# Optimization experiments

Measured on AMD Instinct MI355X. Metric: run time of the kernel, lower is better.

The kernel has to match this reference:

```python
import jax, jax.numpy as jnp
import numpy as np

EPS = 1e-7
BLOCK_SIZE = 128
LN_EPS = 1e-6

def _project(x):
    norm = jnp.maximum(jnp.linalg.norm(x, axis=-1, keepdims=True), EPS)
    max_norm = 1.0 - EPS
    return jnp.where(norm >= 1.0, x / norm * max_norm, x)

def _mobius_add(x, y, c):
    x2 = jnp.sum(x * x, -1, keepdims=True)
    y2 = jnp.sum(y * y, -1, keepdims=True)
    xy = jnp.sum(x * y, -1, keepdims=True)
    num = (1 + 2 * c * xy + c * y2) * x + (1 - c * x2) * y
    den = 1 + 2 * c * xy + c * c * x2 * y2
    return _project(num / jnp.maximum(den, EPS))

def _logmap0(y, c):
    sqrt_c = jnp.maximum(jnp.sqrt(c), EPS)
    y_norm = jnp.linalg.norm(y, axis=-1, keepdims=True)
    safe = jnp.maximum(y_norm, EPS)
    mag = jnp.arctanh(jnp.minimum(y_norm, 1.0 - EPS)) / sqrt_c
    return jnp.where(y_norm < EPS, jnp.zeros_like(y), mag * (y / safe))

def _expmap0(v, c):
    sqrt_c = jnp.maximum(jnp.sqrt(c), EPS)
    v_norm = jnp.linalg.norm(v, axis=-1, keepdims=True)
    safe = jnp.maximum(v_norm, EPS)
    mag = jnp.tanh(sqrt_c * safe) / sqrt_c
    return _project(jnp.where(v_norm < EPS, jnp.zeros_like(v), mag * (v / safe)))

def _dist(x, y, c):
    sqrt_c = jnp.maximum(jnp.sqrt(c), EPS)
    add_norm = jnp.linalg.norm(_mobius_add(-x, y, c), axis=-1)
    sc = jnp.squeeze(sqrt_c, -1)
    arg = jnp.minimum(sc * add_norm, 1.0 - EPS)
    return 2.0 * jnp.arctanh(arg) / sc

def _layernorm(t, scale, bias):
    mu = jnp.mean(t, -1, keepdims=True)
    var = jnp.mean((t - mu) ** 2, -1, keepdims=True)
    return (t - mu) * jax.lax.rsqrt(var + LN_EPS) * scale + bias

def _rope(x, fc):
    # x: [Be, H, bs, hd]; fc: [bs, hd//2] complex
    x_r, x_i = jnp.split(x, 2, -1)
    xc = jax.lax.complex(x_r, x_i)
    rot = xc * fc.reshape(1, 1, fc.shape[0], fc.shape[1])
    return jnp.concatenate([rot.real, rot.imag], -1)

def setup_inputs() -> dict:
    key = jax.random.key(0)
    ks = jax.random.split(key, 8)
    B, N, D, H = 1, 1024, 1024, 16
    w = lambda k, s: jax.random.normal(k, s, jnp.float32) * 0.02
    x = jax.random.normal(ks[0], (B, N, D), jnp.float32) * 0.02  # points inside the ball
    c_global = jax.random.uniform(ks[1], (B, 1), jnp.float32, minval=0.1, maxval=1.0)
    return dict(
        x=x, c_global=c_global,
        qkv_w=w(ks[2], (D, 3 * D)), qkv_b=jnp.zeros((3 * D,), jnp.float32),
        out_w=w(ks[3], (D, D)), out_b=jnp.zeros((D,), jnp.float32),
        ffn_w1=w(ks[4], (D, 4 * D)), ffn_b1=jnp.zeros((4 * D,), jnp.float32),
        ffn_w2=w(ks[5], (4 * D, D)), ffn_b2=jnp.zeros((D,), jnp.float32),
        ln1_scale=jnp.ones((D,), jnp.float32), ln1_bias=jnp.zeros((D,), jnp.float32),
        ln2_scale=jnp.ones((D,), jnp.float32), ln2_bias=jnp.zeros((D,), jnp.float32),
        c_logits=jnp.zeros((H,), jnp.float32),
        geo_scale=jnp.ones((1, H, 1, 1), jnp.float32),
        start_pos=0,
    )

def reference(x, c_global, qkv_w, qkv_b, out_w, out_b, ffn_w1, ffn_b1, ffn_w2, ffn_b2,
              ln1_scale, ln1_bias, ln2_scale, ln2_bias, c_logits, geo_scale, start_pos):
    B, N, D = x.shape
    H = c_logits.shape[0]
    hd = D // H
    bs = BLOCK_SIZE
    nb = N // bs
    Be = B * nb
    xb = x.reshape(Be, bs, D)
    c_b = jnp.repeat(c_global, nb, axis=0).reshape(Be, 1, 1)
    x_res1 = xb
    # tangent-space norm 1 + attention input
    x_norm = _expmap0(_layernorm(_logmap0(xb, c_b), ln1_scale, ln1_bias), c_b)
    x_tan = _logmap0(x_norm, c_b)
    qkv = (x_tan @ qkv_w + qkv_b).reshape(Be, bs, 3, H, hd).transpose(2, 0, 3, 1, 4)
    q, k, v = qkv[0], qkv[1], qkv[2]  # [Be, H, bs, hd]
    # block-local RoPE (module recomputes freqs_cis for h_dim/block_size internally)
    freqs = 1.0 / (10000.0 ** (jnp.arange(0, hd, 2, dtype=jnp.float32) / hd))
    fc = jnp.exp(1j * jnp.outer(jnp.arange(bs), freqs))
    q = _rope(q, fc)
    k = _rope(k, fc)
    c_head = jax.nn.softplus(c_logits).reshape(1, H, 1, 1)
    q_hyp = _expmap0(q, c_head)
    k_hyp = _expmap0(k, c_head)
    d = _dist(q_hyp[:, :, :, None, :], k_hyp[:, :, None, :, :], c_head[:, :, None, :, :])  # [Be,H,bs,bs]
    attn = jax.nn.softmax(-geo_scale * d, axis=-1)
    ao = jnp.einsum('bhqk,bhkd->bhqd', attn, v).transpose(0, 2, 1, 3).reshape(Be, bs, D)
    ao = ao @ out_w + out_b
    x_att = _mobius_add(x_res1, _expmap0(ao, c_b), c_b)
    # tangent-space norm 2 + hyperbolic FFN
    x_norm2 = _expmap0(_layernorm(_logmap0(x_att, c_b), ln2_scale, ln2_bias), c_b)
    t = _logmap0(x_norm2, c_b)
    t = jax.nn.gelu(t @ ffn_w1 + ffn_b1) @ ffn_w2 + ffn_b2
    x_ffn = _expmap0(t, c_b)
    out = _mobius_add(x_att, x_ffn, c_b)
    return out.reshape(B, N, D)
```

## Files before the change

### kernel.cpp

```cpp
#include <hip/hip_runtime.h>

typedef unsigned int uint;
typedef unsigned short ushort;
typedef __attribute__((ext_vector_type(8))) short bf16x8;
typedef __attribute__((ext_vector_type(4))) float f32x4;

#define EPSF 1e-7f
#define ONE_M_EPS 0.99999988079071044921875f
#define ATANH_1ME 8.4056213f
#define Y2_CLIP 0.99999982f

__device__ __forceinline__ ushort f2bf(float f){
  union{float f;uint u;}x; x.f=f; uint u=x.u;
  return (ushort)((u + 0x7fffu + ((u>>16)&1u)) >> 16);
}
__device__ __forceinline__ float bf2f(ushort u){
  union{uint u;float f;}x; x.u = ((uint)u)<<16; return x.f;
}
__device__ __forceinline__ float atanh_c(float a){
  a = fminf(a, ONE_M_EPS);
  return 0.5f*__logf((1.f+a)/(1.f-a));
}
__device__ __forceinline__ float gelu_t(float v){
  return 0.5f*v*(1.f + tanhf(0.7978845608f*(v + 0.044715f*v*v*v)));
}

__device__ __forceinline__ float expmap_factor(float n2, float sc, float& r2){
  float n = sqrtf(n2);
  if (n < EPSF) { r2 = 0.f; return 0.f; }
  float mag = tanhf(sc*n)/sc;
  float f = mag/n;
  if (mag >= 1.f) { f *= ONE_M_EPS/mag; r2 = Y2_CLIP; }
  else r2 = mag*mag;
  return f;
}
__device__ __forceinline__ float roundtrip_factor(float tn2, float sc){
  float tn = sqrtf(tn2);
  if (tn < EPSF) return 0.f;
  float mag = tanhf(sc*tn)/sc;
  if (mag >= 1.f) {
    return ATANH_1ME / (sc * tn);
  } else {
    if (mag < EPSF) return 0.f;
    return (mag/tn) * (atanh_c(mag) / (sc * mag));
  }
}

__device__ __constant__ float FREQS[32] = {
  1.0f, 0.7498942093324559f, 0.5623413251903491f, 0.4216965034285822f,
  0.31622776601683794f, 0.23713737056616552f, 0.1778279410038923f, 0.13335214321633242f,
  0.1f, 0.07498942093324558f, 0.05623413251903491f, 0.04216965034285822f,
  0.03162277660168379f, 0.023713737056616554f, 0.01778279410038923f, 0.013335214321633242f,
  0.01f, 0.007498942093324559f, 0.005623413251903491f, 0.004216965034285822f,
  0.0031622776601683794f, 0.0023713737056616554f, 0.0017782794100389228f, 0.0013335214321633241f,
  0.001f, 0.0007498942093324558f, 0.0005623413251903491f, 0.0004216965034285822f,
  0.00031622776601683794f, 0.00023713737056616553f, 0.00017782794100389227f, 0.00013335214321633243f
};

__device__ __forceinline__ float blkSum(float v, float* tmp){
  #pragma unroll
  for (int o=32;o>0;o>>=1) v += __shfl_xor(v, o, 64);
  int w = threadIdx.x >> 6;
  if ((threadIdx.x & 63) == 0) tmp[w] = v;
  __syncthreads();
  v = tmp[0]+tmp[1]+tmp[2]+tmp[3];
  __syncthreads();
  return v;
}
__device__ __forceinline__ float2 blkSum2(float a, float b, float* tmp){
  #pragma unroll
  for (int o=32;o>0;o>>=1){ a += __shfl_xor(a, o, 64); b += __shfl_xor(b, o, 64); }
  int w = threadIdx.x >> 6;
  if ((threadIdx.x & 63) == 0){ tmp[w] = a; tmp[4+w] = b; }
  __syncthreads();
  float2 r; r.x = tmp[0]+tmp[1]+tmp[2]+tmp[3]; r.y = tmp[4]+tmp[5]+tmp[6]+tmp[7];
  __syncthreads();
  return r;
}

__global__ __launch_bounds__(256) void k_pre(const float* __restrict__ qkv_w,
    const float* __restrict__ out_w, const float* __restrict__ ffn_w1,
    const float* __restrict__ ffn_w2, const float* __restrict__ x,
    const float* __restrict__ cg, const float* __restrict__ lns, const float* __restrict__ lnb,
    ushort* __restrict__ wq, ushort* __restrict__ wo,
    ushort* __restrict__ w1, ushort* __restrict__ w2, ushort* __restrict__ xtan){
  __shared__ float s[32][33];
  int b = blockIdx.x;
  if (b < 12288){
    const float* W; ushort* WT; int K, N;
    if (b < 3072){ W=qkv_w; WT=wq; K=1024; N=3072; }
    else if (b < 4096){ b-=3072; W=out_w; WT=wo; K=1024; N=1024; }
    else if (b < 8192){ b-=4096; W=ffn_w1; WT=w1; K=1024; N=4096; }
    else { b-=8192; W=ffn_w2; WT=w2; K=4096; N=1024; }
    int nbn = N >> 5;
    int n0 = (b % nbn)*32, k0 = (b / nbn)*32;
    int tx = threadIdx.x & 31, ty = threadIdx.x >> 5;
    #pragma unroll
    for (int i=0;i<4;i++)
      s[ty+8*i][tx] = W[(size_t)(k0+ty+8*i)*N + n0+tx];
    __syncthreads();
    #pragma unroll
    for (int i=0;i<4;i++)
      WT[(size_t)(n0+ty+8*i)*K + k0+tx] = f2bf(s[tx][ty+8*i]);
  } else {
    float* tmp = &s[0][0];
    int r = b - 12288, t = threadIdx.x;
    float c = cg[0];
    float sc = fmaxf(sqrtf(c), EPSF);
    float4 xv = ((const float4*)(x + (size_t)r*1024))[t];
    float n2 = blkSum(xv.x*xv.x + xv.y*xv.y + xv.z*xv.z + xv.w*xv.w, tmp);
    float n = sqrtf(n2);
    float f1 = (n < EPSF) ? 0.f : (atanh_c(n) / sc / n);
    float ux = xv.x*f1, uy = xv.y*f1, uz = xv.z*f1, uw = xv.w*f1;
    float2 s12 = blkSum2(ux+uy+uz+uw, ux*ux+uy*uy+uz*uz+uw*uw, tmp);
    float mu = s12.x*(1.f/1024.f);
    float var = s12.y*(1.f/1024.f) - mu*mu;
    float inv = rsqrtf(var + 1e-6f);
    float4 sv = ((const float4*)lns)[t];
    float4 bv = ((const float4*)lnb)[t];
    float ta = (ux-mu)*inv*sv.x + bv.x;
    float tb = (uy-mu)*inv*sv.y + bv.y;
    float tc = (uz-mu)*inv*sv.z + bv.z;
    float td = (uw-mu)*inv*sv.w + bv.w;
    float tn2 = blkSum(ta*ta+tb*tb+tc*tc+td*td, tmp);
    float f = roundtrip_factor(tn2, sc);
    ushort4 o; o.x=f2bf(ta*f); o.y=f2bf(tb*f); o.z=f2bf(tc*f); o.w=f2bf(td*f);
    ((ushort4*)(xtan + (size_t)r*1024))[t] = o;
  }
}

template<int EPI>
__global__ __launch_bounds__(256) void k_gemm(const ushort* __restrict__ A,
    const ushort* __restrict__ Bt, const float* __restrict__ bias,
    void* __restrict__ C, int M, int N, int Kstride, int Kchunk,
    ushort* __restrict__ qhg, ushort* __restrict__ qlg,
    ushort* __restrict__ khg, ushort* __restrict__ klg,
    ushort* __restrict__ vhg, float* __restrict__ q2g, float* __restrict__ k2g,
    const float* __restrict__ clog){
  constexpr int MF = 2, NF = 4;
  __shared__ ushort As[2][128*64];
  __shared__ ushort Bs[2][64*64];
  const int tid = threadIdx.x;
  const int lane = tid & 63;
  const int wid = tid >> 6;
  const int ro = wid * 32;
  const int l15 = lane & 15, hi = lane >> 4;
  const int nwg = gridDim.x * gridDim.y;
  const int lin = blockIdx.y * gridDim.x + blockIdx.x;
  const int qq = nwg >> 3, rr = nwg & 7;
  const int xcd = lin & 7, ii = lin >> 3;
  const int swz = (xcd < rr) ? (xcd*(qq+1) + ii) : (rr*(qq+1) + (xcd-rr)*qq + ii);
  const int m0 = (swz % gridDim.y) * 128;
  const int n0 = (swz / gridDim.y) * 64;
  const int z = blockIdx.z;
  const int kbase = z * Kchunk;
  const int swr = (l15 & 7) << 3;

  f32x4 acc[MF][NF];
  #pragma unroll
  for (int i=0;i<MF;i++)
    #pragma unroll
    for (int j=0;j<NF;j++) acc[i][j] = (f32x4){0.f,0.f,0.f,0.f};

  auto stage = [&](int buf, int koff){
    #pragma unroll
    for (int r2=0;r2<4;r2++){
      int idx = r2*256 + tid;
      int row = idx >> 3, cc = idx & 7;
      int off = koff + ((cc ^ (row & 7)) << 3);
      const ushort* ga = A + (size_t)(m0+row)*Kstride + off;
      int lo = (r2*256 + (tid & 192)) * 8;
      __builtin_amdgcn_global_load_lds((const __attribute__((address_space(1))) uint*)ga,
          (__attribute__((address_space(3))) uint*)&As[buf][lo], 16, 0, 0);
    }
    #pragma unroll
    for (int r2=0;r2<2;r2++){
      int idx = r2*256 + tid;
      int row = idx >> 3, cc = idx & 7;
      int off = koff + ((cc ^ (row & 7)) << 3);
      const ushort* gb = Bt + (size_t)(n0+row)*Kstride + off;
      int lo = (r2*256 + (tid & 192)) * 8;
      __builtin_amdgcn_global_load_lds((const __attribute__((address_space(1))) uint*)gb,
          (__attribute__((address_space(3))) uint*)&Bs[buf][lo], 16, 0, 0);
    }
  };
  auto compute = [&](int buf){
    #pragma unroll
    for (int ks=0;ks<2;ks++){
      bf16x8 af[MF], bfv[NF];
      int cb = (ks*32 + hi*8) ^ swr;
      #pragma unroll
      for (int m2=0;m2<MF;m2++) af[m2]  = *(const bf16x8*)&As[buf][(ro+m2*16+l15)*64 + cb];
      #pragma unroll
      for (int n2=0;n2<NF;n2++) bfv[n2] = *(const bf16x8*)&Bs[buf][(n2*16+l15)*64 + cb];
      #pragma unroll
      for (int m2=0;m2<MF;m2++)
        #pragma unroll
        for (int n2=0;n2<NF;n2++)
          acc[m2][n2] = __builtin_amdgcn_mfma_f32_16x16x32_bf16(af[m2], bfv[n2], acc[m2][n2], 0, 0, 0);
    }
  };

  const int nt = Kchunk >> 6;
  stage(0, kbase);
  __syncthreads();
  int cur = 0;
  for (int t = 1; t < nt; ++t){
    stage(cur ^ 1, kbase + t*64);
    compute(cur);
    __syncthreads();
    cur ^= 1;
  }
  compute(cur);

  if (EPI == 4){
    float v[MF][NF][4];
    #pragma unroll
    for (int m2=0;m2<MF;m2++)
      #pragma unroll
      for (int n2=0;n2<NF;n2++){
        float bb = bias[n0 + n2*16 + l15];
        #pragma unroll
        for (int i=0;i<4;i++) v[m2][n2][i] = acc[m2][n2][i] + bb;
      }
    const int type = n0 >> 10;
    const int h = (n0 & 1023) >> 6;
    if (type < 2){
      #pragma unroll
      for (int m2=0;m2<MF;m2++)
        #pragma unroll
        for (int i=0;i<4;i++){
          int gr = m0 + ro + m2*16 + hi*4 + i;
          float r = (float)(gr & 127);
          #pragma unroll
          for (int pp=0;pp<2;pp++){
            int d = pp*16 + l15;
            float sn, cn; __sincosf(r * FREQS[d], &sn, &cn);
            float a = v[m2][pp][i], b = v[m2][pp+2][i];
            v[m2][pp][i]   = a*cn - b*sn;
            v[m2][pp+2][i] = a*sn + b*cn;
          }
        }
      const float cl = clog[h];
      const float chh = (cl > 20.f) ? cl : log1pf(__expf(cl));
      const float sch = fmaxf(sqrtf(chh), EPSF);
      ushort* hdst = (type==0) ? qhg : khg;
      ushort* ldst = (type==0) ? qlg : klg;
      float*  sdst = (type==0) ? q2g : k2g;
      #pragma unroll
      for (int m2=0;m2<MF;m2++)
        #pragma unroll
        for (int i=0;i<4;i++){
          float n2s = 0.f;
          #pragma unroll
          for (int n2=0;n2<NF;n2++) n2s += v[m2][n2][i]*v[m2][n2][i];
          #pragma unroll
          for (int o=1;o<16;o<<=1) n2s += __shfl_xor(n2s, o);
          float r2; float f = expmap_factor(n2s, sch, r2);
          int gr = m0 + ro + m2*16 + hi*4 + i;
          int be = gr >> 7, r = gr & 127;
          size_t rowbase = ((size_t)(be*16 + h)*128 + r)*64;
          #pragma unroll
          for (int n2=0;n2<NF;n2++){
            float val = v[m2][n2][i]*f;
            ushort hb = f2bf(val);
            ushort lb = f2bf(val - bf2f(hb));
            hdst[rowbase + n2*16 + l15] = hb;
            ldst[rowbase + n2*16 + l15] = lb;
          }
          if (l15 == 0) sdst[(size_t)(be*16+h)*128 + r] = r2;
        }
    } else {
      #pragma unroll
      for (int m2=0;m2<MF;m2++)
        #pragma unroll
        for (int i=0;i<4;i++){
          int gr = m0 + ro + m2*16 + hi*4 + i;
          int be = gr >> 7, r = gr & 127;
          size_t rowbase = ((size_t)(be*16 + h)*128 + r)*64;
          #pragma unroll
          for (int n2=0;n2<NF;n2++)
            vhg[rowbase + n2*16 + l15] = f2bf(v[m2][n2][i]);
        }
    }
    return;
  }

  #pragma unroll
  for (int m=0;m<MF;m++){
    #pragma unroll
    for (int n=0;n<NF;n++){
      int gc = n0 + n*16 + l15;
      float bb = (EPI == 3) ? (z == 0 ? bias[gc] : 0.f) : bias[gc];
      #pragma unroll
      for (int i=0;i<4;i++){
        int gr = m0 + ro + m*16 + hi*4 + i;
        float v2 = acc[m][n][i] + bb;
        if (EPI == 2) v2 = gelu_t(v2);
        if (EPI == 2) ((ushort*)C)[(size_t)gr*N + gc] = f2bf(v2);
        else ((float*)C)[(size_t)z*M*N + (size_t)gr*N + gc] = v2;
      }
    }
  }
}

__global__ __launch_bounds__(256) void k_attn6(const ushort* __restrict__ qhg,
    const ushort* __restrict__ qlg, const ushort* __restrict__ khg,
    const ushort* __restrict__ klg, const ushort* __restrict__ vhg,
    const float* __restrict__ q2g, const float* __restrict__ k2g,
    const float* __restrict__ c_logits, const float* __restrict__ geo,
    ushort* __restrict__ ao){
  __shared__ ushort Kh[128*64], Kl[128*64];
  __shared__ ushort Vth[64*128];
  __shared__ ushort Qh[64*64], Ql[64*64];
  __shared__ float k2s[128], q2s[64];
  const int h = blockIdx.x, be = blockIdx.y, qs = blockIdx.z;
  const int tid = threadIdx.x;
  const float cl = c_logits[h];
  const float ch = (cl > 20.f) ? cl : log1pf(__expf(cl));
  const float sc = fmaxf(sqrtf(ch), EPSF);
  const float gs = geo[h];
  const size_t tbase = (size_t)(be*16 + h)*8192;

  #pragma unroll
  for (int r2=0;r2<4;r2++){
    int idx = r2*256 + tid;
    int row = idx >> 3, cc = idx & 7;
    int off = row*64 + ((cc ^ (row & 7)) << 3);
    int lo = (r2*256 + (tid & 192)) * 8;
    __builtin_amdgcn_global_load_lds((const __attribute__((address_space(1))) uint*)(khg + tbase + off),
        (__attribute__((address_space(3))) uint*)&Kh[lo], 16, 0, 0);
    __builtin_amdgcn_global_load_lds((const __attribute__((address_space(1))) uint*)(klg + tbase + off),
        (__attribute__((address_space(3))) uint*)&Kl[lo], 16, 0, 0);
  }
  #pragma unroll
  for (int r2=0;r2<2;r2++){
    int idx = r2*256 + tid;
    int row = idx >> 3, cc = idx & 7;
    int off = (qs*64 + row)*64 + ((cc ^ (row & 7)) << 3);
    int lo = (r2*256 + (tid & 192)) * 8;
    __builtin_amdgcn_global_load_lds((const __attribute__((address_space(1))) uint*)(qhg + tbase + off),
        (__attribute__((address_space(3))) uint*)&Qh[lo], 16, 0, 0);
    __builtin_amdgcn_global_load_lds((const __attribute__((address_space(1))) uint*)(qlg + tbase + off),
        (__attribute__((address_space(3))) uint*)&Ql[lo], 16, 0, 0);
  }
  if (tid < 128){
    int kv = tid;
    const uint4* src = (const uint4*)(vhg + tbase + kv*64);
    ushort v[64];
    #pragma unroll
    for (int c2=0;c2<8;c2++) *(uint4*)&v[c2*8] = src[c2];
    #pragma unroll
    for (int d=0; d<64; d++){
      int idx = d*128 + (((kv>>3) ^ (d&7))<<3) + (kv&7);
      Vth[idx] = v[d];
    }
    k2s[kv] = k2g[(size_t)(be*16+h)*128 + kv];
  } else if (tid < 192){
    int i2 = tid - 128;
    q2s[i2] = q2g[(size_t)(be*16+h)*128 + qs*64 + i2];
  }
  __syncthreads();

  const int lane = tid & 63, w = tid >> 6;
  const int l15 = lane & 15, hi4 = lane >> 4;
  f32x4 acc[8];
  #pragma unroll
  for (int nf=0;nf<8;nf++) acc[nf] = (f32x4){0.f,0.f,0.f,0.f};
  #pragma unroll
  for (int ks=0; ks<2; ks++){
    int qrowL = w*16 + l15;
    int qidx = qrowL*64 + (((ks*4 + hi4) ^ (qrowL&7))<<3);
    bf16x8 qh = *(const bf16x8*)&Qh[qidx];
    bf16x8 ql2 = *(const bf16x8*)&Ql[qidx];
    #pragma unroll
    for (int nf=0; nf<8; nf++){
      int krow = nf*16 + l15;
      int kidx = krow*64 + (((ks*4 + hi4) ^ (krow&7))<<3);
      bf16x8 kh = *(const bf16x8*)&Kh[kidx];
      bf16x8 kl2 = *(const bf16x8*)&Kl[kidx];
      acc[nf] = __builtin_amdgcn_mfma_f32_16x16x32_bf16(qh, kh, acc[nf], 0, 0, 0);
      acc[nf] = __builtin_amdgcn_mfma_f32_16x16x32_bf16(qh, kl2, acc[nf], 0, 0, 0);
      acc[nf] = __builtin_amdgcn_mfma_f32_16x16x32_bf16(ql2, kh, acc[nf], 0, 0, 0);
    }
  }
  __syncthreads();

  float q2v[4], Bfv[4];
  #pragma unroll
  for (int i=0;i<4;i++){ q2v[i] = q2s[w*16 + hi4*4 + i]; Bfv[i] = 1.f - ch*q2v[i]; }
  const float e2 = 2.f*ch;
  #pragma unroll
  for (int nf=0; nf<8; nf++){
    float k2 = k2s[nf*16 + l15];
    #pragma unroll
    for (int i=0;i<4;i++){
      float xy = acc[nf][i];
      float Af = 1.f + ch*k2 - e2*xy;
      float den = fmaxf(Af - ch*k2*Bfv[i], EPSF);
      float num2 = fmaxf(Af*(Af*q2v[i] - 2.f*Bfv[i]*xy) + Bfv[i]*Bfv[i]*k2, 0.f);
      float rn = sqrtf(num2)/den;
      rn = (rn >= 1.f) ? ONE_M_EPS : rn;
      float arg = fminf(sc*rn, ONE_M_EPS);
      float dd = __logf((1.f+arg)/(1.f-arg)) / sc;
      acc[nf][i] = -gs*dd;
    }
  }
  #pragma unroll
  for (int i=0;i<4;i++){
    float m = acc[0][i];
    #pragma unroll
    for (int nf=1;nf<8;nf++) m = fmaxf(m, acc[nf][i]);
    #pragma unroll
    for (int o=1;o<16;o<<=1) m = fmaxf(m, __shfl_xor(m, o));
    float l = 0.f;
    #pragma unroll
    for (int nf=0;nf<8;nf++){ float pp = __expf(acc[nf][i]-m); acc[nf][i] = pp; l += pp; }
    #pragma unroll
    for (int o=1;o<16;o<<=1) l += __shfl_xor(l, o);
    float inv = 1.f/l;
    #pragma unroll
    for (int nf=0;nf<8;nf++){
      float p = acc[nf][i]*inv;
      ushort ph = f2bf(p);
      ushort pl = f2bf(p - bf2f(ph));
      int row = w*16 + hi4*4 + i, col = nf*16 + l15;
      int idx = row*128 + (((col>>3) ^ (row&7))<<3) + (col&7);
      Kh[idx] = ph; Kl[idx] = pl;
    }
  }
  __syncthreads();

  f32x4 acc2[4];
  #pragma unroll
  for (int nf=0;nf<4;nf++) acc2[nf] = (f32x4){0.f,0.f,0.f,0.f};
  #pragma unroll
  for (int ks=0; ks<4; ks++){
    int prow = w*16 + l15;
    int pidx = prow*128 + (((ks*4 + hi4) ^ (prow&7))<<3);
    bf16x8 ph = *(const bf16x8*)&Kh[pidx];
    bf16x8 pl = *(const bf16x8*)&Kl[pidx];
    #pragma unroll
    for (int nf=0; nf<4; nf++){
      int vrow = nf*16 + l15;
      int vidx = vrow*128 + (((ks*4 + hi4) ^ (vrow&7))<<3);
      bf16x8 vh = *(const bf16x8*)&Vth[vidx];
      acc2[nf] = __builtin_amdgcn_mfma_f32_16x16x32_bf16(ph, vh, acc2[nf], 0, 0, 0);
      acc2[nf] = __builtin_amdgcn_mfma_f32_16x16x32_bf16(pl, vh, acc2[nf], 0, 0, 0);
    }
  }
  #pragma unroll
  for (int nf=0; nf<4; nf++)
    #pragma unroll
    for (int i=0;i<4;i++){
      int row = qs*64 + w*16 + hi4*4 + i;
      int col = nf*16 + l15;
      ao[(size_t)(be*128 + row)*1024 + h*64 + col] = f2bf(acc2[nf][i]);
    }
}

__global__ __launch_bounds__(256) void k_postattn(const float* __restrict__ x,
    const float* __restrict__ proj, const float* __restrict__ cg,
    const float* __restrict__ lns, const float* __restrict__ lnb,
    float* __restrict__ xatt, ushort* __restrict__ tout){
  __shared__ float tmp[8];
  int r = blockIdx.x, t = threadIdx.x;
  float c = cg[0], sc = fmaxf(sqrtf(c), EPSF);
  float4 pa = ((const float4*)(proj + (size_t)r*1024))[t];
  float4 pb = ((const float4*)(proj + 1024*1024 + (size_t)r*1024))[t];
  float4 pc = ((const float4*)(proj + 2*1024*1024 + (size_t)r*1024))[t];
  float4 pd = ((const float4*)(proj + 3*1024*1024 + (size_t)r*1024))[t];
  float4 pv; pv.x=(pa.x+pb.x)+(pc.x+pd.x); pv.y=(pa.y+pb.y)+(pc.y+pd.y);
  pv.z=(pa.z+pb.z)+(pc.z+pd.z); pv.w=(pa.w+pb.w)+(pc.w+pd.w);
  float4 xv = ((const float4*)(x + (size_t)r*1024))[t];
  float pn2 = blkSum(pv.x*pv.x+pv.y*pv.y+pv.z*pv.z+pv.w*pv.w, tmp);
  float y2; float fy = expmap_factor(pn2, sc, y2);
  float ya = pv.x*fy, yb = pv.y*fy, yc = pv.z*fy, yd = pv.w*fy;
  float2 s = blkSum2(xv.x*xv.x+xv.y*xv.y+xv.z*xv.z+xv.w*xv.w,
                     xv.x*ya+xv.y*yb+xv.z*yc+xv.w*yd, tmp);
  float x2 = s.x, xy = s.y;
  float Af = 1.f + 2.f*c*xy + c*y2;
  float Bf = 1.f - c*x2;
  float den = fmaxf(1.f + 2.f*c*xy + c*c*x2*y2, EPSF);
  float num2 = fmaxf(Af*Af*x2 + 2.f*Af*Bf*xy + Bf*Bf*y2, 0.f);
  float rn = sqrtf(num2)/den;
  float fp = (rn >= 1.f) ? (ONE_M_EPS/fmaxf(rn,EPSF)) : 1.f;
  float xan = (rn >= 1.f) ? ONE_M_EPS : rn;
  float g = fp/den;
  float xa = (Af*xv.x + Bf*ya)*g;
  float xb = (Af*xv.y + Bf*yb)*g;
  float xc = (Af*xv.z + Bf*yc)*g;
  float xd = (Af*xv.w + Bf*yd)*g;
  float4 xo; xo.x=xa; xo.y=xb; xo.z=xc; xo.w=xd;
  ((float4*)(xatt + (size_t)r*1024))[t] = xo;
  float at = (rn >= 1.f) ? ATANH_1ME : atanh_c(xan);
  float fl = (xan < EPSF) ? 0.f : at / sc / fmaxf(xan, EPSF);
  float ux = xa*fl, uy = xb*fl, uz = xc*fl, uw = xd*fl;
  float2 s12 = blkSum2(ux+uy+uz+uw, ux*ux+uy*uy+uz*uz+uw*uw, tmp);
  float mu = s12.x*(1.f/1024.f);
  float var = s12.y*(1.f/1024.f) - mu*mu;
  float inv = rsqrtf(var + 1e-6f);
  float4 sv = ((const float4*)lns)[t];
  float4 bv = ((const float4*)lnb)[t];
  float ta = (ux-mu)*inv*sv.x + bv.x;
  float tb = (uy-mu)*inv*sv.y + bv.y;
  float tc = (uz-mu)*inv*sv.z + bv.z;
  float td = (uw-mu)*inv*sv.w + bv.w;
  float tn2 = blkSum(ta*ta+tb*tb+tc*tc+td*td, tmp);
  float f = roundtrip_factor(tn2, sc);
  ushort4 o; o.x=f2bf(ta*f); o.y=f2bf(tb*f); o.z=f2bf(tc*f); o.w=f2bf(td*f);
  ((ushort4*)(tout + (size_t)r*1024))[t] = o;
}

__global__ __launch_bounds__(256) void k_final(const float* __restrict__ xatt,
    const float* __restrict__ tf, const float* __restrict__ cg, float* __restrict__ out){
  __shared__ float tmp[8];
  int r = blockIdx.x, t = threadIdx.x;
  float c = cg[0], sc = fmaxf(sqrtf(c), EPSF);
  float4 fa = ((const float4*)(tf + (size_t)r*1024))[t];
  float4 fb = ((const float4*)(tf + 1024*1024 + (size_t)r*1024))[t];
  float4 fc = ((const float4*)(tf + 2*1024*1024 + (size_t)r*1024))[t];
  float4 fd = ((const float4*)(tf + 3*1024*1024 + (size_t)r*1024))[t];
  float4 fv; fv.x=(fa.x+fb.x)+(fc.x+fd.x); fv.y=(fa.y+fb.y)+(fc.y+fd.y);
  fv.z=(fa.z+fb.z)+(fc.z+fd.z); fv.w=(fa.w+fb.w)+(fc.w+fd.w);
  float4 xv = ((const float4*)(xatt + (size_t)r*1024))[t];
  float fn2 = blkSum(fv.x*fv.x+fv.y*fv.y+fv.z*fv.z+fv.w*fv.w, tmp);
  float y2; float fy = expmap_factor(fn2, sc, y2);
  float ya = fv.x*fy, yb = fv.y*fy, yc = fv.z*fy, yd = fv.w*fy;
  float2 s = blkSum2(xv.x*xv.x+xv.y*xv.y+xv.z*xv.z+xv.w*xv.w,
                     xv.x*ya+xv.y*yb+xv.z*yc+xv.w*yd, tmp);
  float x2 = s.x, xy = s.y;
  float Af = 1.f + 2.f*c*xy + c*y2;
  float Bf = 1.f - c*x2;
  float den = fmaxf(1.f + 2.f*c*xy + c*c*x2*y2, EPSF);
  float num2 = fmaxf(Af*Af*x2 + 2.f*Af*Bf*xy + Bf*Bf*y2, 0.f);
  float rn = sqrtf(num2)/den;
  float fp = (rn >= 1.f) ? (ONE_M_EPS/fmaxf(rn,EPSF)) : 1.f;
  float g = fp/den;
  float4 o;
  o.x = (Af*xv.x + Bf*ya)*g;
  o.y = (Af*xv.y + Bf*yb)*g;
  o.z = (Af*xv.z + Bf*yc)*g;
  o.w = (Af*xv.w + Bf*yd)*g;
  ((float4*)(out + (size_t)r*1024))[t] = o;
}

extern "C" void kernel_launch(void* const* d_in, const int* in_sizes, int n_in,
                              void* d_out, int out_size, void* d_ws, size_t ws_size,
                              hipStream_t stream){
  (void)in_sizes; (void)n_in; (void)out_size; (void)ws_size;
  const float* x     = (const float*)d_in[0];
  const float* cg    = (const float*)d_in[1];
  const float* qkv_w = (const float*)d_in[2];
  const float* qkv_b = (const float*)d_in[3];
  const float* out_w = (const float*)d_in[4];
  const float* out_b = (const float*)d_in[5];
  const float* ffn_w1= (const float*)d_in[6];
  const float* ffn_b1= (const float*)d_in[7];
  const float* ffn_w2= (const float*)d_in[8];
  const float* ffn_b2= (const float*)d_in[9];
  const float* ln1s  = (const float*)d_in[10];
  const float* ln1b  = (const float*)d_in[11];
  const float* ln2s  = (const float*)d_in[12];
  const float* ln2b  = (const float*)d_in[13];
  const float* clog  = (const float*)d_in[14];
  const float* geo   = (const float*)d_in[15];

  char* p = (char*)d_ws;
  auto take = [&](size_t n){ char* r = p; p += (n + 255) & ~(size_t)255; return r; };
  ushort* wt_qkv  = (ushort*)take((size_t)3072*1024*2);
  ushort* wt_out  = (ushort*)take((size_t)1024*1024*2);
  ushort* wt_ffn1 = (ushort*)take((size_t)4096*1024*2);
  ushort* wt_ffn2 = (ushort*)take((size_t)1024*4096*2);
  float*  bufA    = (float*)take((size_t)1024*4096*4);
  ushort* bufB    = (ushort*)take((size_t)1024*1024*2);
  float*  bufC    = (float*)take((size_t)4*1024*1024*4);
  float*  xatt    = (float*)take((size_t)1024*1024*4);
  ushort* tbuf    = (ushort*)take((size_t)1024*1024*2);
  ushort* qhg     = (ushort*)take((size_t)1024*1024*2);
  ushort* qlg     = (ushort*)take((size_t)1024*1024*2);
  ushort* khg     = (ushort*)take((size_t)1024*1024*2);
  ushort* klg     = (ushort*)take((size_t)1024*1024*2);
  ushort* vhg     = (ushort*)take((size_t)1024*1024*2);
  float*  q2g     = (float*)take((size_t)16384*4);
  float*  k2g     = (float*)take((size_t)16384*4);

  k_pre<<<13312, 256, 0, stream>>>(qkv_w, out_w, ffn_w1, ffn_w2, x, cg, ln1s, ln1b,
                                   wt_qkv, wt_out, wt_ffn1, wt_ffn2, bufB);
  k_gemm<4><<<dim3(48,8,1), 256, 0, stream>>>(bufB, wt_qkv, qkv_b, nullptr, 1024, 3072, 1024, 1024,
                                              qhg, qlg, khg, klg, vhg, q2g, k2g, clog);
  k_attn6<<<dim3(16,8,2), 256, 0, stream>>>(qhg, qlg, khg, klg, vhg, q2g, k2g, clog, geo, bufB);
  k_gemm<3><<<dim3(16,8,4), 256, 0, stream>>>(bufB, wt_out, out_b, (void*)bufC, 1024, 1024, 1024, 256,
                                              nullptr,nullptr,nullptr,nullptr,nullptr,nullptr,nullptr,nullptr);
  k_postattn<<<1024, 256, 0, stream>>>(x, bufC, cg, ln2s, ln2b, xatt, tbuf);
  k_gemm<2><<<dim3(64,8,1), 256, 0, stream>>>(tbuf, wt_ffn1, ffn_b1, (void*)bufA, 1024, 4096, 1024, 1024,
                                              nullptr,nullptr,nullptr,nullptr,nullptr,nullptr,nullptr,nullptr);
  k_gemm<3><<<dim3(16,8,4), 256, 0, stream>>>((const ushort*)bufA, wt_ffn2, ffn_b2, (void*)bufC, 1024, 1024, 4096, 1024,
                                              nullptr,nullptr,nullptr,nullptr,nullptr,nullptr,nullptr,nullptr);
  k_final<<<1024, 256, 0, stream>>>(xatt, bufC, cg, (float*)d_out);
}
```

Measured before the change: 121.4 us.

## Unfuse QKV epilogue into split-K GEMM plus separate RoPE/expmap prep kernel

Replaces the fused QKV GEMM epilogue (RoPE, expmap, hi/lo bf16 split) with a split-K=2 GEMM that writes fp32 partials, followed by a new row-wise kernel that sums the partials and applies RoPE, expmap and the bf16 split. The aim is to double the number of workgroups for the QKV GEMM (384 to 768) so the GPU is better occupied. The cost is an extra kernel launch and a round trip of a 2x1024x3072 fp32 buffer through memory, which is why the workspace buffer is enlarged.

```diff
diff --git a/kernel.cpp b/kernel.cpp
--- a/kernel.cpp
+++ b/kernel.cpp
@@ -132,11 +132,7 @@
 template<int EPI>
 __global__ __launch_bounds__(256) void k_gemm(const ushort* __restrict__ A,
     const ushort* __restrict__ Bt, const float* __restrict__ bias,
-    void* __restrict__ C, int M, int N, int Kstride, int Kchunk,
-    ushort* __restrict__ qhg, ushort* __restrict__ qlg,
-    ushort* __restrict__ khg, ushort* __restrict__ klg,
-    ushort* __restrict__ vhg, float* __restrict__ q2g, float* __restrict__ k2g,
-    const float* __restrict__ clog){
+    void* __restrict__ C, int M, int N, int Kstride, int Kchunk){
   constexpr int MF = 2, NF = 4;
   __shared__ ushort As[2][128*64];
   __shared__ ushort Bs[2][64*64];
@@ -213,79 +209,6 @@
   }
   compute(cur);
 
-  if (EPI == 4){
-    float v[MF][NF][4];
-    #pragma unroll
-    for (int m2=0;m2<MF;m2++)
-      #pragma unroll
-      for (int n2=0;n2<NF;n2++){
-        float bb = bias[n0 + n2*16 + l15];
-        #pragma unroll
-        for (int i=0;i<4;i++) v[m2][n2][i] = acc[m2][n2][i] + bb;
-      }
-    const int type = n0 >> 10;
-    const int h = (n0 & 1023) >> 6;
-    if (type < 2){
-      #pragma unroll
-      for (int m2=0;m2<MF;m2++)
-        #pragma unroll
-        for (int i=0;i<4;i++){
-          int gr = m0 + ro + m2*16 + hi*4 + i;
-          float r = (float)(gr & 127);
-          #pragma unroll
-          for (int pp=0;pp<2;pp++){
-            int d = pp*16 + l15;
-            float sn, cn; __sincosf(r * FREQS[d], &sn, &cn);
-            float a = v[m2][pp][i], b = v[m2][pp+2][i];
-            v[m2][pp][i]   = a*cn - b*sn;
-            v[m2][pp+2][i] = a*sn + b*cn;
-          }
-        }
-      const float cl = clog[h];
-      const float chh = (cl > 20.f) ? cl : log1pf(__expf(cl));
-      const float sch = fmaxf(sqrtf(chh), EPSF);
-      ushort* hdst = (type==0) ? qhg : khg;
-      ushort* ldst = (type==0) ? qlg : klg;
-      float*  sdst = (type==0) ? q2g : k2g;
-      #pragma unroll
-      for (int m2=0;m2<MF;m2++)
-        #pragma unroll
-        for (int i=0;i<4;i++){
-          float n2s = 0.f;
-          #pragma unroll
-          for (int n2=0;n2<NF;n2++) n2s += v[m2][n2][i]*v[m2][n2][i];
-          #pragma unroll
-          for (int o=1;o<16;o<<=1) n2s += __shfl_xor(n2s, o);
-          float r2; float f = expmap_factor(n2s, sch, r2);
-          int gr = m0 + ro + m2*16 + hi*4 + i;
-          int be = gr >> 7, r = gr & 127;
-          size_t rowbase = ((size_t)(be*16 + h)*128 + r)*64;
-          #pragma unroll
-          for (int n2=0;n2<NF;n2++){
-            float val = v[m2][n2][i]*f;
-            ushort hb = f2bf(val);
-            ushort lb = f2bf(val - bf2f(hb));
-            hdst[rowbase + n2*16 + l15] = hb;
-            ldst[rowbase + n2*16 + l15] = lb;
-          }
-          if (l15 == 0) sdst[(size_t)(be*16+h)*128 + r] = r2;
-        }
-    } else {
-      #pragma unroll
-      for (int m2=0;m2<MF;m2++)
-        #pragma unroll
-        for (int i=0;i<4;i++){
-          int gr = m0 + ro + m2*16 + hi*4 + i;
-          int be = gr >> 7, r = gr & 127;
-          size_t rowbase = ((size_t)(be*16 + h)*128 + r)*64;
-          #pragma unroll
-          for (int n2=0;n2<NF;n2++)
-            vhg[rowbase + n2*16 + l15] = f2bf(v[m2][n2][i]);
-        }
-    }
-    return;
-  }
-
   #pragma unroll
   for (int m=0;m<MF;m++){
     #pragma unroll
@@ -295,12 +218,70 @@
       #pragma unroll
       for (int i=0;i<4;i++){
         int gr = m0 + ro + m*16 + hi*4 + i;
-        float v2 = acc[m][n][i] + bb;
-        if (EPI == 2) v2 = gelu_t(v2);
-        if (EPI == 2) ((ushort*)C)[(size_t)gr*N + gc] = f2bf(v2);
-        else ((float*)C)[(size_t)z*M*N + (size_t)gr*N + gc] = v2;
+        float v = acc[m][n][i] + bb;
+        if (EPI == 2) v = gelu_t(v);
+        if (EPI == 2) ((ushort*)C)[(size_t)gr*N + gc] = f2bf(v);
+        else ((float*)C)[(size_t)z*M*N + (size_t)gr*N + gc] = v;
       }
     }
+  }
+}
+
+__global__ __launch_bounds__(256) void k_qkvprep(const float* __restrict__ qkv,
+    const float* __restrict__ clog,
+    ushort* __restrict__ qhg, ushort* __restrict__ qlg,
+    ushort* __restrict__ khg, ushort* __restrict__ klg,
+    ushort* __restrict__ vhg, float* __restrict__ q2g, float* __restrict__ k2g){
+  constexpr size_t PSTRIDE = (size_t)1024*3072;
+  const int gr = blockIdx.x;
+  const int be = gr >> 7, r = gr & 127;
+  const int t = threadIdx.x;
+  const int h = t >> 4, d = t & 15;
+  const float cl = clog[h];
+  const float ch = (cl > 20.f) ? cl : log1pf(__expf(cl));
+  const float sc = fmaxf(sqrtf(ch), EPSF);
+  const float* base  = qkv + (size_t)gr*3072 + h*64;
+  const float* base2 = base + PSTRIDE;
+  const size_t rowbase = ((size_t)(be*16 + h)*128 + r)*64;
+  const float fr = (float)r;
+  #pragma unroll
+  for (int qk=0; qk<2; qk++){
+    int off = qk*1024;
+    float v0 = base[off+d]    + base2[off+d];
+    float v1 = base[off+d+16] + base2[off+d+16];
+    float v2 = base[off+d+32] + base2[off+d+32];
+    float v3 = base[off+d+48] + base2[off+d+48];
+    float sn, cn;
+    __sincosf(fr * FREQS[d], &sn, &cn);
+    float a = v0, b = v2;
+    v0 = a*cn - b*sn; v2 = a*sn + b*cn;
+    __sincosf(fr * FREQS[d+16], &sn, &cn);
+    a = v1; b = v3;
+    v1 = a*cn - b*sn; v3 = a*sn + b*cn;
+    float n2 = v0*v0 + v1*v1 + v2*v2 + v3*v3;
+    #pragma unroll
+    for (int o=1;o<16;o<<=1) n2 += __shfl_xor(n2, o);
+    float r2; float f = expmap_factor(n2, sc, r2);
+    ushort* hd = qk ? khg : qhg;
+    ushort* ld = qk ? klg : qlg;
+    float val;
+    val = v0*f; ushort h0 = f2bf(val), l0 = f2bf(val - bf2f(h0));
+    val = v1*f; ushort h1 = f2bf(val), l1 = f2bf(val - bf2f(h1));
+    val = v2*f; ushort h2 = f2bf(val), l2 = f2bf(val - bf2f(h2));
+    val = v3*f; ushort h3 = f2bf(val), l3 = f2bf(val - bf2f(h3));
+    hd[rowbase+d]=h0; hd[rowbase+d+16]=h1; hd[rowbase+d+32]=h2; hd[rowbase+d+48]=h3;
+    ld[rowbase+d]=l0; ld[rowbase+d+16]=l1; ld[rowbase+d+32]=l2; ld[rowbase+d+48]=l3;
+    if (d == 0) (qk ? k2g : q2g)[(size_t)(be*16+h)*128 + r] = r2;
+  }
+  {
+    float v0 = base[2048+d]    + base2[2048+d];
+    float v1 = base[2048+d+16] + base2[2048+d+16];
+    float v2 = base[2048+d+32] + base2[2048+d+32];
+    float v3 = base[2048+d+48] + base2[2048+d+48];
+    vhg[rowbase+d]    = f2bf(v0);
+    vhg[rowbase+d+16] = f2bf(v1);
+    vhg[rowbase+d+32] = f2bf(v2);
+    vhg[rowbase+d+48] = f2bf(v3);
   }
 }
 
@@ -572,7 +553,7 @@
   ushort* wt_out  = (ushort*)take((size_t)1024*1024*2);
   ushort* wt_ffn1 = (ushort*)take((size_t)4096*1024*2);
   ushort* wt_ffn2 = (ushort*)take((size_t)1024*4096*2);
-  float*  bufA    = (float*)take((size_t)1024*4096*4);
+  float*  bufA    = (float*)take((size_t)2*1024*3072*4);
   ushort* bufB    = (ushort*)take((size_t)1024*1024*2);
   float*  bufC    = (float*)take((size_t)4*1024*1024*4);
   float*  xatt    = (float*)take((size_t)1024*1024*4);
@@ -587,15 +568,12 @@
 
   k_pre<<<13312, 256, 0, stream>>>(qkv_w, out_w, ffn_w1, ffn_w2, x, cg, ln1s, ln1b,
                                    wt_qkv, wt_out, wt_ffn1, wt_ffn2, bufB);
-  k_gemm<4><<<dim3(48,8,1), 256, 0, stream>>>(bufB, wt_qkv, qkv_b, nullptr, 1024, 3072, 1024, 1024,
-                                              qhg, qlg, khg, klg, vhg, q2g, k2g, clog);
+  k_gemm<3><<<dim3(48,8,2), 256, 0, stream>>>(bufB, wt_qkv, qkv_b, (void*)bufA, 1024, 3072, 1024, 512);
+  k_qkvprep<<<1024, 256, 0, stream>>>(bufA, clog, qhg, qlg, khg, klg, vhg, q2g, k2g);
   k_attn6<<<dim3(16,8,2), 256, 0, stream>>>(qhg, qlg, khg, klg, vhg, q2g, k2g, clog, geo, bufB);
-  k_gemm<3><<<dim3(16,8,4), 256, 0, stream>>>(bufB, wt_out, out_b, (void*)bufC, 1024, 1024, 1024, 256,
-                                              nullptr,nullptr,nullptr,nullptr,nullptr,nullptr,nullptr,nullptr);
+  k_gemm<3><<<dim3(16,8,4), 256, 0, stream>>>(bufB, wt_out, out_b, (void*)bufC, 1024, 1024, 1024, 256);
   k_postattn<<<1024, 256, 0, stream>>>(x, bufC, cg, ln2s, ln2b, xatt, tbuf);
-  k_gemm<2><<<dim3(64,8,1), 256, 0, stream>>>(tbuf, wt_ffn1, ffn_b1, (void*)bufA, 1024, 4096, 1024, 1024,
-                                              nullptr,nullptr,nullptr,nullptr,nullptr,nullptr,nullptr,nullptr);
-  k_gemm<3><<<dim3(16,8,4), 256, 0, stream>>>((const ushort*)bufA, wt_ffn2, ffn_b2, (void*)bufC, 1024, 1024, 4096, 1024,
-                                              nullptr,nullptr,nullptr,nullptr,nullptr,nullptr,nullptr,nullptr);
+  k_gemm<2><<<dim3(64,8,1), 256, 0, stream>>>(tbuf, wt_ffn1, ffn_b1, (void*)bufA, 1024, 4096, 1024, 1024);
+  k_gemm<3><<<dim3(16,8,4), 256, 0, stream>>>((const ushort*)bufA, wt_ffn2, ffn_b2, (void*)bufC, 1024, 1024, 4096, 1024);
   k_final<<<1024, 256, 0, stream>>>(xatt, bufC, cg, (float*)d_out);
 }
```

Measured after the change: 117.6 us. 1.03x faster.
